# Kernel optimization log

Hardware: AMD Instinct MI355X
Metric: run time of the kernel (lower is better)

The kernel has to match this reference:

```python
import jax, jax.numpy as jnp
import numpy as np

L, C, S = 4096, 128, 64
SAMPLE_RATE = 4096.0  # Hz; dt offset is 1/sample_rate as in the flax module


def setup_inputs() -> dict:
    key = jax.random.key(0)
    ks = jax.random.split(key, 4)
    x = jax.random.normal(ks[0], (L, C), dtype=jnp.float32)
    # S4D-real init: A = -arange(1, S+1), param stores log(-A) broadcast to (C, S)
    A_log = jnp.broadcast_to(
        jnp.log(jnp.arange(1, S + 1, dtype=jnp.float32)), (C, S)
    )
    sc = 1.0 / np.sqrt(C)  # lecun_normal-like scale for Dense kernels
    B_kernel = (jax.random.normal(ks[1], (C, S)) * sc).astype(jnp.float32)
    B_bias = jnp.zeros((S,), jnp.float32)
    C_kernel = (jax.random.normal(ks[2], (C, S)) * sc).astype(jnp.float32)
    C_bias = jnp.zeros((S,), jnp.float32)
    dt_kernel = (jax.random.normal(ks[3], (C, C)) * sc).astype(jnp.float32)
    dt_bias = jnp.zeros((C,), jnp.float32)
    return {
        "x": x,
        "A_log": A_log,
        "B_kernel": B_kernel,
        "B_bias": B_bias,
        "C_kernel": C_kernel,
        "C_bias": C_bias,
        "dt_kernel": dt_kernel,
        "dt_bias": dt_bias,
    }


def reference(x, A_log, B_kernel, B_bias, C_kernel, C_bias, dt_kernel, dt_bias):
    # ssm params
    A = -jnp.exp(A_log)                                   # (C, S), negative real
    B = 1.0 + x @ B_kernel + B_bias                       # (L, S)
    Cm = x @ C_kernel + C_bias                            # (L, S)
    dt = jax.nn.softplus(1.0 / SAMPLE_RATE + x @ dt_kernel + dt_bias)  # (L, C)
    # discretization (ZOH for diagonal real A)
    At = jnp.exp(A[None, :, :] * dt[:, :, None])          # (L, C, S)
    ut = (At - 1.0) * (B[:, None, :] / A[None, :, :]) * x[:, :, None]  # (L, C, S)

    # parallel linear-recurrence scan: h_t = At_t * h_{t-1} + ut_t, h0 = 0
    def comb(e1, e2):
        a1, u1 = e1
        a2, u2 = e2
        return (a2 * a1, a2 * u1 + u2)

    _, ht = jax.lax.associative_scan(comb, (At, ut))      # scans over axis 0 (L)
    y = jnp.einsum("ls,lcs->lc", Cm, ht)                  # (L, C)
    return y
```

## Files before the change

kernel.cpp:

```cpp
#include <hip/hip_runtime.h>
#include <math.h>

#define LL 4096
#define CC 128
#define SS 64
#define CLEN 32
#define GW 8
#define NG 16
#define CS 8192
#define LOG2E 1.44269504088896f

__global__ __launch_bounds__(256) void k_proj(
    const float* __restrict__ x,
    const float* __restrict__ Bk, const float* __restrict__ Bb,
    const float* __restrict__ Ck, const float* __restrict__ Cb,
    const float* __restrict__ Dk, const float* __restrict__ Db,
    float* __restrict__ Bmat, float* __restrict__ Cmat,
    float* __restrict__ DTmT, float* __restrict__ xT)
{
    __shared__ float xs[CC][20];
    const int r0 = blockIdx.x * 16;
    const int t = threadIdx.x;
    {
        const int r = t >> 4, k8 = (t & 15) * 8;
        const float4 v0 = *(const float4*)&x[(r0 + r) * CC + k8];
        const float4 v1 = *(const float4*)&x[(r0 + r) * CC + k8 + 4];
        xs[k8+0][r] = v0.x; xs[k8+1][r] = v0.y; xs[k8+2][r] = v0.z; xs[k8+3][r] = v0.w;
        xs[k8+4][r] = v1.x; xs[k8+5][r] = v1.y; xs[k8+6][r] = v1.z; xs[k8+7][r] = v1.w;
    }
    __syncthreads();
    {
        const int k = t >> 1, half = (t & 1) * 8;
        const float4 a = *(const float4*)&xs[k][half];
        const float4 b = *(const float4*)&xs[k][half + 4];
        *(float4*)&xT[k * LL + r0 + half]     = a;
        *(float4*)&xT[k * LL + r0 + half + 4] = b;
    }
    const int tc = t & 63, tr = t >> 6;
    const float* Wb; int wstride, wo;
    if (tc < 16)      { Wb = Bk; wstride = SS; wo = 4 * tc; }
    else if (tc < 32) { Wb = Ck; wstride = SS; wo = 4 * tc - 64; }
    else              { Wb = Dk; wstride = CC; wo = 4 * tc - 128; }
    float acc[4][4];
#pragma unroll
    for (int r = 0; r < 4; ++r)
#pragma unroll
        for (int j = 0; j < 4; ++j) acc[r][j] = 0.0f;
    for (int k = 0; k < CC; ++k) {
        const float4 wq = *(const float4*)(Wb + k * wstride + wo);
        const float4 xq = *(const float4*)&xs[k][4 * tr];
        const float wv[4] = {wq.x, wq.y, wq.z, wq.w};
        const float xv[4] = {xq.x, xq.y, xq.z, xq.w};
#pragma unroll
        for (int r = 0; r < 4; ++r)
#pragma unroll
            for (int j = 0; j < 4; ++j) acc[r][j] = fmaf(xv[r], wv[j], acc[r][j]);
    }
    const int rb = r0 + 4 * tr;
    if (tc < 32) {
        const float* bb = (tc < 16) ? Bb : Cb;
        const float add = (tc < 16) ? 1.0f : 0.0f;
        float bias[4];
#pragma unroll
        for (int j = 0; j < 4; ++j) bias[j] = add + bb[wo + j];
        float* dst = (tc < 16) ? Bmat : Cmat;
#pragma unroll
        for (int r = 0; r < 4; ++r) {
            const float4 o = make_float4(acc[r][0] + bias[0], acc[r][1] + bias[1],
                                         acc[r][2] + bias[2], acc[r][3] + bias[3]);
            *(float4*)&dst[(rb + r) * SS + wo] = o;
        }
    } else {
#pragma unroll
        for (int j = 0; j < 4; ++j) {
            const float bj = Db[wo + j] + 0.000244140625f;
            float sp[4];
#pragma unroll
            for (int r = 0; r < 4; ++r) {
                const float z = acc[r][j] + bj;
                sp[r] = fmaxf(z, 0.0f) + log1pf(__expf(-fabsf(z)));
            }
            *(float4*)&DTmT[(wo + j) * LL + rb] = make_float4(sp[0], sp[1], sp[2], sp[3]);
        }
    }
}

__global__ __launch_bounds__(512, 4) void k_sweep1(
    const float* __restrict__ xT, const float* __restrict__ A_log,
    const float* __restrict__ Bmat, const float* __restrict__ DTmT,
    float2* __restrict__ GaGu)
{
    __shared__ float2 agg[GW][SS];
    const int lane = threadIdx.x & 63;
    const int w = __builtin_amdgcn_readfirstlane(threadIdx.x >> 6);
    const int c = blockIdx.x >> 4;
    const int g = blockIdx.x & (NG - 1);
    const int j = c * SS + lane;
    const float A = -__expf(A_log[j]);
    const float A2 = A * LOG2E;
    const float invA = 1.0f / A;
    const int l0 = (g * GW + w) * CLEN;
    const float* dtp = DTmT + c * LL + l0;
    const float* xp  = xT   + c * LL + l0;
    const float* Bp  = Bmat + l0 * SS + lane;
    float ap = 1.0f, uc = 0.0f;
#pragma unroll
    for (int i = 0; i < CLEN; ++i) {
        const float At = __builtin_amdgcn_exp2f(A2 * dtp[i]);
        const float u  = (At - 1.0f) * invA * (Bp[i * SS] * xp[i]);
        ap *= At;
        uc = fmaf(At, uc, u);
    }
    agg[w][lane] = make_float2(ap, uc);
    __syncthreads();
    if (w == 0) {
        float ga = 1.0f, gu = 0.0f;
#pragma unroll
        for (int k = 0; k < GW; ++k) {
            const float2 t = agg[k][lane];
            gu = fmaf(t.x, gu, t.y);
            ga *= t.x;
        }
        GaGu[g * CS + j] = make_float2(ga, gu);
    }
}

__global__ __launch_bounds__(512, 4) void k_emit(
    const float* __restrict__ xT, const float* __restrict__ A_log,
    const float* __restrict__ Bmat, const float* __restrict__ Cmat,
    const float* __restrict__ DTmT,
    const float2* __restrict__ GaGu,
    float* __restrict__ y)
{
    __shared__ float2 agg[GW][SS];
    __shared__ float hgs[SS];
    const int lane = threadIdx.x & 63;
    const int w = __builtin_amdgcn_readfirstlane(threadIdx.x >> 6);
    const int c = blockIdx.x >> 4;
    const int g = blockIdx.x & (NG - 1);
    const int j = c * SS + lane;
    const float A = -__expf(A_log[j]);
    const float A2 = A * LOG2E;
    const float invA = 1.0f / A;
    if (w == 0) {
        float hg = 0.0f;
        float2 ggr[NG - 1];
#pragma unroll
        for (int gg = 0; gg < NG - 1; ++gg) ggr[gg] = GaGu[gg * CS + j];
#pragma unroll
        for (int gg = 0; gg < NG - 1; ++gg)
            hg = (gg < g) ? fmaf(ggr[gg].x, hg, ggr[gg].y) : hg;
        hgs[lane] = hg;
    }
    const int l0 = (g * GW + w) * CLEN;
    const float* dtp = DTmT + c * LL + l0;
    const float* xp  = xT   + c * LL + l0;
    const float* Bp  = Bmat + l0 * SS + lane;
    const float* Cp  = Cmat + l0 * SS + lane;
    float at[CLEN], uu[CLEN];
    {
        float ap = 1.0f, uc = 0.0f;
#pragma unroll
        for (int i = 0; i < CLEN; ++i) {
            at[i] = __builtin_amdgcn_exp2f(A2 * dtp[i]);
            uu[i] = (at[i] - 1.0f) * invA * (Bp[i * SS] * xp[i]);
            ap *= at[i];
            uc = fmaf(at[i], uc, uu[i]);
        }
        agg[w][lane] = make_float2(ap, uc);
    }
    __syncthreads();
    const float hg = hgs[lane];
    float ea = 1.0f, eu = 0.0f;
    for (int k = 0; k < w; ++k) {
        const float2 t = agg[k][lane];
        eu = fmaf(t.x, eu, t.y);
        ea *= t.x;
    }
    float h = fmaf(ea, hg, eu);
#pragma unroll
    for (int i = 0; i < CLEN; ++i) {
        h = fmaf(at[i], h, uu[i]);
        uu[i] = Cp[i * SS] * h;
    }
#pragma unroll
    for (int k = 0; k < 5; ++k) {
        const int d = 1 << k;
        const bool hi = (lane & d) != 0;
#pragma unroll
        for (int i2 = 0; i2 < (CLEN >> (k + 1)); ++i2) {
            const float a = uu[2 * i2], b = uu[2 * i2 + 1];
            const float send = hi ? a : b;
            const float t = __shfl_xor(send, d, 64);
            uu[i2] = (hi ? b : a) + t;
        }
    }
    const float t = __shfl_xor(uu[0], 32, 64);
    const float yv = uu[0] + t;
    if (lane < 32) y[(l0 + lane) * CC + c] = yv;
}

extern "C" void kernel_launch(void* const* d_in, const int* in_sizes, int n_in,
                              void* d_out, int out_size, void* d_ws, size_t ws_size,
                              hipStream_t stream)
{
    const float* x  = (const float*)d_in[0];
    const float* Al = (const float*)d_in[1];
    const float* Bk = (const float*)d_in[2];
    const float* Bb = (const float*)d_in[3];
    const float* Ck = (const float*)d_in[4];
    const float* Cb = (const float*)d_in[5];
    const float* Dk = (const float*)d_in[6];
    const float* Db = (const float*)d_in[7];
    float* y  = (float*)d_out;
    float* ws = (float*)d_ws;

    float*  Bmat = ws;
    float*  Cmat = Bmat + LL * SS;
    float*  DTmT = Cmat + LL * SS;
    float*  xT   = DTmT + CC * LL;
    float2* GaGu = (float2*)(xT + CC * LL);

    k_proj  <<<LL / 16, 256, 0, stream>>>(x, Bk, Bb, Ck, Cb, Dk, Db, Bmat, Cmat, DTmT, xT);
    k_sweep1<<<CC * NG, 512, 0, stream>>>(xT, Al, Bmat, DTmT, GaGu);
    k_emit  <<<CC * NG, 512, 0, stream>>>(xT, Al, Bmat, Cmat, DTmT, GaGu, y);
}
```

Baseline: 47.18 us.

## Split projection kernel into single-wave blocks per output group, drop shared-memory staging

The projection kernel is restructured from 256 blocks of 256 threads into 1024 single-wavefront blocks, each computing one 64-column output group (B, C, or one half of dt) for a 16-row stripe. x is read directly from global memory in 8-wide k chunks instead of being staged and transposed in LDS, which removes the __syncthreads. The xT transpose is now written by the cg==0 blocks from registers. This aims for more parallel blocks and no barrier, at the cost of four blocks each re-reading the same x rows and of uncoalesced strided x loads.

Measured after the change: 51.68 us. 1.1x slower.

```diff
diff --git a/kernel.cpp b/kernel.cpp
--- a/kernel.cpp
+++ b/kernel.cpp
@@ -10,7 +10,7 @@
 #define CS 8192
 #define LOG2E 1.44269504088896f
 
-__global__ __launch_bounds__(256) void k_proj(
+__global__ __launch_bounds__(64) void k_proj(
     const float* __restrict__ x,
     const float* __restrict__ Bk, const float* __restrict__ Bb,
     const float* __restrict__ Ck, const float* __restrict__ Cb,
@@ -18,52 +18,65 @@
     float* __restrict__ Bmat, float* __restrict__ Cmat,
     float* __restrict__ DTmT, float* __restrict__ xT)
 {
-    __shared__ float xs[CC][20];
-    const int r0 = blockIdx.x * 16;
-    const int t = threadIdx.x;
-    {
-        const int r = t >> 4, k8 = (t & 15) * 8;
-        const float4 v0 = *(const float4*)&x[(r0 + r) * CC + k8];
-        const float4 v1 = *(const float4*)&x[(r0 + r) * CC + k8 + 4];
-        xs[k8+0][r] = v0.x; xs[k8+1][r] = v0.y; xs[k8+2][r] = v0.z; xs[k8+3][r] = v0.w;
-        xs[k8+4][r] = v1.x; xs[k8+5][r] = v1.y; xs[k8+6][r] = v1.z; xs[k8+7][r] = v1.w;
-    }
-    __syncthreads();
-    {
-        const int k = t >> 1, half = (t & 1) * 8;
-        const float4 a = *(const float4*)&xs[k][half];
-        const float4 b = *(const float4*)&xs[k][half + 4];
-        *(float4*)&xT[k * LL + r0 + half]     = a;
-        *(float4*)&xT[k * LL + r0 + half + 4] = b;
-    }
-    const int tc = t & 63, tr = t >> 6;
-    const float* Wb; int wstride, wo;
-    if (tc < 16)      { Wb = Bk; wstride = SS; wo = 4 * tc; }
-    else if (tc < 32) { Wb = Ck; wstride = SS; wo = 4 * tc - 64; }
-    else              { Wb = Dk; wstride = CC; wo = 4 * tc - 128; }
+    const int b = blockIdx.x;
+    const int stripe = b >> 2, cg = b & 3;
+    const int r0 = stripe * 16;
+    const int lane = threadIdx.x;
+    const int cq = lane & 15, rq = lane >> 4;
+    const int rb = r0 + 4 * rq;
+    const float* W; int wstr, wo;
+    if (cg == 0)      { W = Bk; wstr = SS; wo = 4 * cq; }
+    else if (cg == 1) { W = Ck; wstr = SS; wo = 4 * cq; }
+    else if (cg == 2) { W = Dk; wstr = CC; wo = 4 * cq; }
+    else              { W = Dk; wstr = CC; wo = 64 + 4 * cq; }
+
     float acc[4][4];
 #pragma unroll
     for (int r = 0; r < 4; ++r)
 #pragma unroll
         for (int j = 0; j < 4; ++j) acc[r][j] = 0.0f;
-    for (int k = 0; k < CC; ++k) {
-        const float4 wq = *(const float4*)(Wb + k * wstride + wo);
-        const float4 xq = *(const float4*)&xs[k][4 * tr];
-        const float wv[4] = {wq.x, wq.y, wq.z, wq.w};
-        const float xv[4] = {xq.x, xq.y, xq.z, xq.w};
-#pragma unroll
-        for (int r = 0; r < 4; ++r)
-#pragma unroll
-            for (int j = 0; j < 4; ++j) acc[r][j] = fmaf(xv[r], wv[j], acc[r][j]);
-    }
-    const int rb = r0 + 4 * tr;
-    if (tc < 32) {
-        const float* bb = (tc < 16) ? Bb : Cb;
-        const float add = (tc < 16) ? 1.0f : 0.0f;
+
+    for (int it = 0; it < 16; ++it) {
+        const int k8 = it * 8;
+        float4 wv[8];
+#pragma unroll
+        for (int i = 0; i < 8; ++i)
+            wv[i] = *(const float4*)(W + (k8 + i) * wstr + wo);
+        float xf[4][8];
+#pragma unroll
+        for (int r = 0; r < 4; ++r) {
+            const float4 a  = *(const float4*)&x[(rb + r) * CC + k8];
+            const float4 b2 = *(const float4*)&x[(rb + r) * CC + k8 + 4];
+            xf[r][0] = a.x;  xf[r][1] = a.y;  xf[r][2] = a.z;  xf[r][3] = a.w;
+            xf[r][4] = b2.x; xf[r][5] = b2.y; xf[r][6] = b2.z; xf[r][7] = b2.w;
+        }
+#pragma unroll
+        for (int i = 0; i < 8; ++i) {
+            const float4 wq = wv[i];
+#pragma unroll
+            for (int r = 0; r < 4; ++r) {
+                acc[r][0] = fmaf(xf[r][i], wq.x, acc[r][0]);
+                acc[r][1] = fmaf(xf[r][i], wq.y, acc[r][1]);
+                acc[r][2] = fmaf(xf[r][i], wq.z, acc[r][2]);
+                acc[r][3] = fmaf(xf[r][i], wq.w, acc[r][3]);
+            }
+        }
+        if (cg == 0 && cq == it) {
+#pragma unroll
+            for (int i = 0; i < 8; ++i) {
+                *(float4*)&xT[(k8 + i) * LL + rb] =
+                    make_float4(xf[0][i], xf[1][i], xf[2][i], xf[3][i]);
+            }
+        }
+    }
+
+    if (cg < 2) {
+        const float* bb = (cg == 0) ? Bb : Cb;
+        const float add = (cg == 0) ? 1.0f : 0.0f;
+        float* dst = (cg == 0) ? Bmat : Cmat;
         float bias[4];
 #pragma unroll
         for (int j = 0; j < 4; ++j) bias[j] = add + bb[wo + j];
-        float* dst = (tc < 16) ? Bmat : Cmat;
 #pragma unroll
         for (int r = 0; r < 4; ++r) {
             const float4 o = make_float4(acc[r][0] + bias[0], acc[r][1] + bias[1],
@@ -221,7 +234,7 @@
     float*  xT   = DTmT + CC * LL;
     float2* GaGu = (float2*)(xT + CC * LL);
 
-    k_proj  <<<LL / 16, 256, 0, stream>>>(x, Bk, Bb, Ck, Cb, Dk, Db, Bmat, Cmat, DTmT, xT);
+    k_proj  <<<1024,    64,  0, stream>>>(x, Bk, Bb, Ck, Cb, Dk, Db, Bmat, Cmat, DTmT, xT);
     k_sweep1<<<CC * NG, 512, 0, stream>>>(xT, Al, Bmat, DTmT, GaGu);
     k_emit  <<<CC * NG, 512, 0, stream>>>(xT, Al, Bmat, Cmat, DTmT, GaGu, y);
 }
```
